# Performance work log

Measured on AMD Instinct MI355X. Metric: run time of the kernel, lower is better.

## Reference

```python
import jax, jax.numpy as jnp
import numpy as np

N_NODES = 200000
N_EDGES = 3200000
N_GRAPHS = 4096
IN_CH = 78
H1, H2, OUT_DIM = 64, 128, 128


def setup_inputs() -> dict:
    key = jax.random.key(0)
    ks = jax.random.split(key, 10)
    x = jax.random.normal(ks[0], (N_NODES, IN_CH), dtype=jnp.float32)
    edge_index = jax.random.randint(ks[1], (2, N_EDGES), 0, N_NODES, dtype=jnp.int64)
    batch = jnp.sort(jax.random.randint(ks[2], (N_NODES,), 0, N_GRAPHS, dtype=jnp.int64))
    # GCNConv weights (PyG: lin has no bias by default; conv bias added after aggregation)
    def glorot(k, fan_in, fan_out):
        lim = jnp.sqrt(6.0 / (fan_in + fan_out)).astype(jnp.float32)
        return jax.random.uniform(k, (fan_in, fan_out), jnp.float32, -lim, lim)
    W1 = glorot(ks[3], IN_CH, H1)
    b1 = jnp.zeros((H1,), jnp.float32)
    W2 = glorot(ks[4], H1, H2)
    b2 = jnp.zeros((H2,), jnp.float32)
    fc_w = glorot(ks[5], H2, OUT_DIM)
    fc_b = jnp.zeros((OUT_DIM,), jnp.float32)
    return {"x": x, "edge_index": edge_index, "batch": batch,
            "W1": W1, "b1": b1, "W2": W2, "b2": b2, "fc_w": fc_w, "fc_b": fc_b}


def _gcn_forward(x, edge_index, batch, W1, b1, W2, b2, fc_w, fc_b):
    N = x.shape[0]
    # GCNConv default: add self loops, symmetric deg^-1/2 normalization
    self_loops = jnp.arange(N, dtype=edge_index.dtype)
    src = jnp.concatenate([edge_index[0], self_loops])  # [E+N]
    dst = jnp.concatenate([edge_index[1], self_loops])  # [E+N]
    deg = jax.ops.segment_sum(jnp.ones_like(dst, dtype=jnp.float32), dst,
                              num_segments=N)  # in-degree incl self loop
    dinv = jnp.where(deg > 0, jax.lax.rsqrt(jnp.maximum(deg, 1.0)), 0.0)
    norm = dinv[src] * dinv[dst]  # [E+N]

    def gcn_layer(h, W, b):
        hw = h @ W                              # transform first (small dims)
        msg = hw[src] * norm[:, None]           # gather + scale  [E+N, F]
        agg = jax.ops.segment_sum(msg, dst, num_segments=N)  # scatter-add
        return agg + b

    h = jax.nn.relu(gcn_layer(x, W1, b1))
    h = jax.nn.relu(gcn_layer(h, W2, b2))
    # global_mean_pool over per-graph segments
    counts = jax.ops.segment_sum(jnp.ones((N,), jnp.float32), batch,
                                 num_segments=N_GRAPHS)
    pooled = jax.ops.segment_sum(h, batch, num_segments=N_GRAPHS)
    pooled = pooled / jnp.maximum(counts, 1.0)[:, None]  # [G, H2]
    return pooled @ fc_w + fc_b                           # [G, OUT_DIM]


def reference(x, edge_index, batch, W1, b1, W2, b2, fc_w, fc_b):
    return _gcn_forward(x, edge_index, batch, W1, b1, W2, b2, fc_w, fc_b)
```

## Files before the change

kernel.cpp:

```cpp
#include <hip/hip_runtime.h>
#include <hip/hip_bf16.h>

#define NN 200000
#define NE 3200000
#define NG 4096
#define INC 78
#define C1 64
#define C2 128
#define ODIM 128
#define KP1 96

#define BSZ 256
#define NBKT 782
#define NBLK 196
#define EPB 16327
#define SCN (NBKT*NBLK)

using bf16 = __hip_bfloat16;
typedef __attribute__((ext_vector_type(8))) short bf16x8;
typedef __attribute__((ext_vector_type(4))) float f32x4;

static inline size_t alignup(size_t x) { return (x + 255) & ~size_t(255); }

__device__ __forceinline__ float bflo(unsigned u) { return __uint_as_float(u << 16); }
__device__ __forceinline__ float bfhi(unsigned u) { return __uint_as_float(u & 0xffff0000u); }
__device__ __forceinline__ unsigned short f2bf(float f) {
    __hip_bfloat16 h = __float2bfloat16(f);
    return *reinterpret_cast<unsigned short*>(&h);
}

__global__ void hist1_kernel(const int* __restrict__ dst, int* __restrict__ histM) {
    __shared__ int lh[NBKT];
    for (int j = threadIdx.x; j < NBKT; j += 256) lh[j] = 0;
    __syncthreads();
    int e0 = blockIdx.x * EPB;
    int e1 = e0 + EPB; if (e1 > NE) e1 = NE;
    for (int e = e0 + threadIdx.x; e < e1; e += 256)
        atomicAdd(&lh[((unsigned)dst[e]) >> 8], 1);
    __syncthreads();
    for (int j = threadIdx.x; j < NBKT; j += 256)
        histM[j * NBLK + blockIdx.x] = lh[j];
}

__global__ void scan1_kernel(int* __restrict__ data, int* __restrict__ bsum, int n) {
    __shared__ int tmp[256];
    int tid = threadIdx.x, gid = blockIdx.x * 256 + tid;
    int v = (gid < n) ? data[gid] : 0;
    tmp[tid] = v;
    __syncthreads();
    for (int off = 1; off < 256; off <<= 1) {
        int t = (tid >= off) ? tmp[tid - off] : 0;
        __syncthreads();
        tmp[tid] += t;
        __syncthreads();
    }
    if (gid < n) data[gid] = tmp[tid] - v;
    if (tid == 255) bsum[blockIdx.x] = tmp[255];
}

__global__ void scan2_kernel(int* __restrict__ bsum, int nb) {
    __shared__ int tmp[1024];
    int tid = threadIdx.x;
    int v = (tid < nb) ? bsum[tid] : 0;
    tmp[tid] = v;
    __syncthreads();
    for (int off = 1; off < 1024; off <<= 1) {
        int t = (tid >= off) ? tmp[tid - off] : 0;
        __syncthreads();
        tmp[tid] += t;
        __syncthreads();
    }
    if (tid < nb) bsum[tid] = tmp[tid] - v;
}

__global__ void scatter2_kernel(const int* __restrict__ src, const int* __restrict__ dst,
                                const int* __restrict__ histM, const int* __restrict__ bsum,
                                unsigned* __restrict__ ebuf) {
    __shared__ int lc[NBKT];
    for (int j = threadIdx.x; j < NBKT; j += 256) {
        int idx = j * NBLK + blockIdx.x;
        lc[j] = histM[idx] + bsum[idx >> 8];
    }
    __syncthreads();
    int e0 = blockIdx.x * EPB;
    int e1 = e0 + EPB; if (e1 > NE) e1 = NE;
    for (int e = e0 + threadIdx.x; e < e1; e += 256) {
        int d = dst[e];
        int s = src[e];
        int pos = atomicAdd(&lc[((unsigned)d) >> 8], 1);
        ebuf[pos] = ((unsigned)s << 8) | (unsigned)(d & 255);
    }
}

__global__ __launch_bounds__(256) void degcsr_kernel(
    const unsigned* __restrict__ ebuf, const int* __restrict__ histM,
    const int* __restrict__ bsum, int* __restrict__ rs, float* __restrict__ dinv,
    unsigned* __restrict__ csr) {
    __shared__ int cnt[BSZ];
    __shared__ int pfx[BSZ];
    int b = blockIdx.x;
    int i0 = b * NBLK;
    int s0 = histM[i0] + bsum[i0 >> 8];
    int s1 = NE;
    if (b + 1 < NBKT) {
        int i1 = (b + 1) * NBLK;
        s1 = histM[i1] + bsum[i1 >> 8];
    }
    cnt[threadIdx.x] = 0;
    __syncthreads();
    for (int i = s0 + threadIdx.x; i < s1; i += 256)
        atomicAdd(&cnt[ebuf[i] & 255], 1);
    __syncthreads();
    int v = cnt[threadIdx.x];
    pfx[threadIdx.x] = v;
    __syncthreads();
    for (int off = 1; off < 256; off <<= 1) {
        int t = (threadIdx.x >= off) ? pfx[threadIdx.x - off] : 0;
        __syncthreads();
        pfx[threadIdx.x] += t;
        __syncthreads();
    }
    int myrs = s0 + pfx[threadIdx.x] - v;
    int node = b * BSZ + threadIdx.x;
    if (node < NN) {
        rs[node] = myrs;
        dinv[node] = rsqrtf((float)v + 1.0f);
    }
    if (node == NN) rs[NN] = NE;
    __syncthreads();
    cnt[threadIdx.x] = 0;
    pfx[threadIdx.x] = myrs;
    __syncthreads();
    for (int i = s0 + threadIdx.x; i < s1; i += 256) {
        unsigned rec = ebuf[i];
        int nl = rec & 255;
        int pos = atomicAdd(&cnt[nl], 1);
        csr[pfx[nl] + pos] = rec >> 8;
    }
}

__global__ void convw2_kernel(const float* __restrict__ W1, const float* __restrict__ W2,
                              unsigned short* __restrict__ Wt1, unsigned short* __restrict__ Wt2) {
    int idx = blockIdx.x * 256 + threadIdx.x;
    if (idx < C1 * KP1) {
        int c = idx / KP1, k = idx % KP1;
        Wt1[idx] = f2bf((k < INC) ? W1[k * C1 + c] : 0.f);
    } else {
        int j = idx - C1 * KP1;
        if (j < C2 * C1) {
            int c = j / C1, k = j % C1;
            Wt2[j] = f2bf(W2[k * C2 + c]);
        }
    }
}

__global__ __launch_bounds__(256) void gemm1_mfma(const float* __restrict__ x,
                                                  const unsigned short* __restrict__ Wt1,
                                                  const float* __restrict__ dinv,
                                                  unsigned short* __restrict__ hw1s) {
    int wave = threadIdx.x >> 6, lane = threadIdx.x & 63;
    int r = lane & 15, kg = lane >> 4;
    int row0 = blockIdx.x * 64 + wave * 16;
    const float* arow = x + (size_t)(row0 + r) * INC;
    bf16x8 a[3];
    #pragma unroll
    for (int t = 0; t < 3; ++t) {
        union { bf16x8 v; unsigned short u[8]; } tmp;
        #pragma unroll
        for (int j = 0; j < 8; ++j) {
            int k = t * 32 + kg * 8 + j;
            tmp.u[j] = (k < INC) ? f2bf(arow[k]) : (unsigned short)0;
        }
        a[t] = tmp.v;
    }
    float dsc[4];
    #pragma unroll
    for (int i = 0; i < 4; ++i) dsc[i] = dinv[row0 + kg * 4 + i];
    #pragma unroll
    for (int nt = 0; nt < 4; ++nt) {
        const unsigned short* wrow = Wt1 + (size_t)(nt * 16 + r) * KP1 + kg * 8;
        bf16x8 b0 = *(const bf16x8*)(wrow);
        bf16x8 b1 = *(const bf16x8*)(wrow + 32);
        bf16x8 b2 = *(const bf16x8*)(wrow + 64);
        f32x4 acc = {0.f, 0.f, 0.f, 0.f};
        acc = __builtin_amdgcn_mfma_f32_16x16x32_bf16(a[0], b0, acc, 0, 0, 0);
        acc = __builtin_amdgcn_mfma_f32_16x16x32_bf16(a[1], b1, acc, 0, 0, 0);
        acc = __builtin_amdgcn_mfma_f32_16x16x32_bf16(a[2], b2, acc, 0, 0, 0);
        unsigned short* cb = hw1s + (size_t)(row0 + kg * 4) * C1 + nt * 16 + r;
        #pragma unroll
        for (int i = 0; i < 4; ++i) cb[(size_t)i * C1] = f2bf(acc[i] * dsc[i]);
    }
}

template <int EP>
__global__ __launch_bounds__(256) void agg_csr_kernel(
    const unsigned* __restrict__ csr, const int* __restrict__ rs,
    const float* __restrict__ dinv, const unsigned short* __restrict__ vin,
    const float* __restrict__ bias, unsigned short* __restrict__ vout) {
    int node = blockIdx.x * 32 + (threadIdx.x >> 3);
    int l = threadIdx.x & 7;
    int c0 = l * 8;
    int start = rs[node], len = rs[node + 1] - start;
    float a0 = 0.f, a1 = 0.f, a2 = 0.f, a3 = 0.f;
    float a4 = 0.f, a5 = 0.f, a6 = 0.f, a7 = 0.f;
    int e = 0;
    for (; e + 2 <= len; e += 2) {
        unsigned sA = csr[start + e], sB = csr[start + e + 1];
        uint4 ra = *(const uint4*)(vin + (size_t)sA * 64 + c0);
        uint4 rb = *(const uint4*)(vin + (size_t)sB * 64 + c0);
        a0 += bflo(ra.x) + bflo(rb.x);
        a1 += bfhi(ra.x) + bfhi(rb.x);
        a2 += bflo(ra.y) + bflo(rb.y);
        a3 += bfhi(ra.y) + bfhi(rb.y);
        a4 += bflo(ra.z) + bflo(rb.z);
        a5 += bfhi(ra.z) + bfhi(rb.z);
        a6 += bflo(ra.w) + bflo(rb.w);
        a7 += bfhi(ra.w) + bfhi(rb.w);
    }
    if (e < len) {
        unsigned sA = csr[start + e];
        uint4 ra = *(const uint4*)(vin + (size_t)sA * 64 + c0);
        a0 += bflo(ra.x); a1 += bfhi(ra.x);
        a2 += bflo(ra.y); a3 += bfhi(ra.y);
        a4 += bflo(ra.z); a5 += bfhi(ra.z);
        a6 += bflo(ra.w); a7 += bfhi(ra.w);
    }
    uint4 sv = *(const uint4*)(vin + (size_t)node * 64 + c0);
    a0 += bflo(sv.x); a1 += bfhi(sv.x);
    a2 += bflo(sv.y); a3 += bfhi(sv.y);
    a4 += bflo(sv.z); a5 += bfhi(sv.z);
    a6 += bflo(sv.w); a7 += bfhi(sv.w);
    float d = dinv[node];
    a0 *= d; a1 *= d; a2 *= d; a3 *= d; a4 *= d; a5 *= d; a6 *= d; a7 *= d;
    if (EP == 1) {
        a0 = fmaxf(a0 + bias[c0 + 0], 0.f) * d;
        a1 = fmaxf(a1 + bias[c0 + 1], 0.f) * d;
        a2 = fmaxf(a2 + bias[c0 + 2], 0.f) * d;
        a3 = fmaxf(a3 + bias[c0 + 3], 0.f) * d;
        a4 = fmaxf(a4 + bias[c0 + 4], 0.f) * d;
        a5 = fmaxf(a5 + bias[c0 + 5], 0.f) * d;
        a6 = fmaxf(a6 + bias[c0 + 6], 0.f) * d;
        a7 = fmaxf(a7 + bias[c0 + 7], 0.f) * d;
    }
    uint4 o;
    o.x = (unsigned)f2bf(a0) | ((unsigned)f2bf(a1) << 16);
    o.y = (unsigned)f2bf(a2) | ((unsigned)f2bf(a3) << 16);
    o.z = (unsigned)f2bf(a4) | ((unsigned)f2bf(a5) << 16);
    o.w = (unsigned)f2bf(a6) | ((unsigned)f2bf(a7) << 16);
    *(uint4*)(vout + (size_t)node * 64 + c0) = o;
}

__global__ __launch_bounds__(256) void gemm2_mfma(const unsigned short* __restrict__ aggH,
                                                  const unsigned short* __restrict__ Wt2,
                                                  const float* __restrict__ b2,
                                                  unsigned short* __restrict__ h2) {
    int wave = threadIdx.x >> 6, lane = threadIdx.x & 63;
    int r = lane & 15, kg = lane >> 4;
    int row0 = blockIdx.x * 64 + wave * 16;
    const unsigned short* arow = aggH + (size_t)(row0 + r) * 64 + kg * 8;
    bf16x8 a0 = *(const bf16x8*)(arow);
    bf16x8 a1 = *(const bf16x8*)(arow + 32);
    #pragma unroll
    for (int nt = 0; nt < 8; ++nt) {
        const unsigned short* wrow = Wt2 + (size_t)(nt * 16 + r) * C1 + kg * 8;
        bf16x8 b0 = *(const bf16x8*)(wrow);
        bf16x8 b1 = *(const bf16x8*)(wrow + 32);
        f32x4 acc = {0.f, 0.f, 0.f, 0.f};
        acc = __builtin_amdgcn_mfma_f32_16x16x32_bf16(a0, b0, acc, 0, 0, 0);
        acc = __builtin_amdgcn_mfma_f32_16x16x32_bf16(a1, b1, acc, 0, 0, 0);
        int col = nt * 16 + r;
        float bb = b2[col];
        unsigned short* cb = h2 + (size_t)(row0 + kg * 4) * C2 + col;
        #pragma unroll
        for (int i = 0; i < 4; ++i) cb[(size_t)i * C2] = f2bf(fmaxf(acc[i] + bb, 0.f));
    }
}

__device__ __forceinline__ int lbound(const int* __restrict__ a, int n, int key) {
    int lo = 0, hi = n;
    while (lo < hi) {
        int mid = (lo + hi) >> 1;
        if (a[mid] < key) lo = mid + 1; else hi = mid;
    }
    return lo;
}

__global__ __launch_bounds__(256) void pool_fc_kernel(const unsigned short* __restrict__ h2,
                                                      const int* __restrict__ batch,
                                                      const float* __restrict__ fcw,
                                                      const float* __restrict__ fcb,
                                                      float* __restrict__ out) {
    __shared__ float ps[512];
    __shared__ float pr[128];
    int g = blockIdx.x;
    int lo = lbound(batch, NN, g);
    int hi = lbound(batch, NN, g + 1);
    int cnt = hi - lo;
    int rg = threadIdx.x >> 6;
    int p = threadIdx.x & 63;
    float s0 = 0.f, s1 = 0.f;
    for (int r = lo + rg; r < hi; r += 4) {
        unsigned v = *(const unsigned*)(h2 + (size_t)r * C2 + p * 2);
        s0 += bflo(v);
        s1 += bfhi(v);
    }
    ps[threadIdx.x * 2 + 0] = s0;
    ps[threadIdx.x * 2 + 1] = s1;
    __syncthreads();
    if (threadIdx.x < 64) {
        float inv = 1.0f / (float)((cnt > 0) ? cnt : 1);
        int t = threadIdx.x;
        float r0 = 0.f, r1 = 0.f;
        #pragma unroll
        for (int k = 0; k < 4; ++k) {
            r0 += ps[(k * 64 + t) * 2 + 0];
            r1 += ps[(k * 64 + t) * 2 + 1];
        }
        pr[2 * t + 0] = r0 * inv;
        pr[2 * t + 1] = r1 * inv;
    }
    __syncthreads();
    if (threadIdx.x < 128) {
        int o = threadIdx.x;
        float acc = fcb[o];
        #pragma unroll 8
        for (int k = 0; k < C2; ++k) acc += pr[k] * fcw[k * ODIM + o];
        out[(size_t)g * ODIM + o] = acc;
    }
}

extern "C" void kernel_launch(void* const* d_in, const int* in_sizes, int n_in,
                              void* d_out, int out_size, void* d_ws, size_t ws_size,
                              hipStream_t stream) {
    const float* x   = (const float*)d_in[0];
    const int*   ei  = (const int*)d_in[1];
    const int*   bat = (const int*)d_in[2];
    const float* W1  = (const float*)d_in[3];
    const float* b1  = (const float*)d_in[4];
    const float* W2  = (const float*)d_in[5];
    const float* b2  = (const float*)d_in[6];
    const float* fcw = (const float*)d_in[7];
    const float* fcb = (const float*)d_in[8];
    float* out = (float*)d_out;

    const int* src = ei;
    const int* dst = ei + NE;

    char* ws = (char*)d_ws;
    int* histM   = (int*)ws;            ws += alignup((size_t)SCN * 4);
    int* bsum    = (int*)ws;            ws += alignup(1024 * 4);
    int* rs      = (int*)ws;            ws += alignup((size_t)(NN + 1) * 4);
    float* dinv  = (float*)ws;          ws += alignup((size_t)NN * 4);
    unsigned short* Wt1 = (unsigned short*)ws;  ws += alignup((size_t)C1 * KP1 * 2);
    unsigned short* Wt2 = (unsigned short*)ws;  ws += alignup((size_t)C2 * C1 * 2);
    unsigned short* hw1s = (unsigned short*)ws; ws += alignup((size_t)NN * C1 * 2);
    unsigned short* aggH = hw1s;
    unsigned* ebuf = (unsigned*)ws;     ws += alignup((size_t)NE * 4);
    unsigned* csr  = (unsigned*)ws;     ws += alignup((size_t)NE * 4);
    unsigned short* h1s = (unsigned short*)ws;  ws += alignup((size_t)NN * C1 * 2);
    unsigned short* h2 = (unsigned short*)ebuf;

    hist1_kernel<<<NBLK, 256, 0, stream>>>(dst, histM);
    const int SCB = (SCN + 255) / 256;
    scan1_kernel<<<SCB, 256, 0, stream>>>(histM, bsum, SCN);
    scan2_kernel<<<1, 1024, 0, stream>>>(bsum, SCB);
    scatter2_kernel<<<NBLK, 256, 0, stream>>>(src, dst, histM, bsum, ebuf);

    degcsr_kernel<<<NBKT, 256, 0, stream>>>(ebuf, histM, bsum, rs, dinv, csr);

    convw2_kernel<<<(C1 * KP1 + C2 * C1 + 255) / 256, 256, 0, stream>>>(W1, W2, Wt1, Wt2);

    gemm1_mfma<<<NN / 64, 256, 0, stream>>>(x, Wt1, dinv, hw1s);
    agg_csr_kernel<1><<<NN / 32, 256, 0, stream>>>(csr, rs, dinv, hw1s, b1, h1s);

    agg_csr_kernel<2><<<NN / 32, 256, 0, stream>>>(csr, rs, dinv, h1s, b1, aggH);
    gemm2_mfma<<<NN / 64, 256, 0, stream>>>(aggH, Wt2, b2, h2);

    pool_fc_kernel<<<NG, 256, 0, stream>>>(h2, bat, fcw, fcb, out);
}
```

Before: 304.4 us.

## Fuse layer-2 aggregation into GEMM, build CSR in place, stage x via LDS

```diff
diff --git a/kernel.cpp b/kernel.cpp
--- a/kernel.cpp
+++ b/kernel.cpp
@@ -15,6 +15,7 @@
 #define NBLK 196
 #define EPB 16327
 #define SCN (NBKT*NBLK)
+#define MAXREC 12288
 
 using bf16 = __hip_bfloat16;
 typedef __attribute__((ext_vector_type(8))) short bf16x8;
@@ -75,7 +76,7 @@
 
 __global__ void scatter2_kernel(const int* __restrict__ src, const int* __restrict__ dst,
                                 const int* __restrict__ histM, const int* __restrict__ bsum,
-                                unsigned* __restrict__ ebuf) {
+                                unsigned* __restrict__ ecsr) {
     __shared__ int lc[NBKT];
     for (int j = threadIdx.x; j < NBKT; j += 256) {
         int idx = j * NBLK + blockIdx.x;
@@ -88,16 +89,16 @@
         int d = dst[e];
         int s = src[e];
         int pos = atomicAdd(&lc[((unsigned)d) >> 8], 1);
-        ebuf[pos] = ((unsigned)s << 8) | (unsigned)(d & 255);
+        ecsr[pos] = ((unsigned)s << 8) | (unsigned)(d & 255);
     }
 }
 
 __global__ __launch_bounds__(256) void degcsr_kernel(
-    const unsigned* __restrict__ ebuf, const int* __restrict__ histM,
-    const int* __restrict__ bsum, int* __restrict__ rs, float* __restrict__ dinv,
-    unsigned* __restrict__ csr) {
+    const int* __restrict__ histM, const int* __restrict__ bsum,
+    int* __restrict__ rs, float* __restrict__ dinv, unsigned* __restrict__ ecsr) {
     __shared__ int cnt[BSZ];
     __shared__ int pfx[BSZ];
+    __shared__ unsigned recs[MAXREC];
     int b = blockIdx.x;
     int i0 = b * NBLK;
     int s0 = histM[i0] + bsum[i0 >> 8];
@@ -106,10 +107,13 @@
         int i1 = (b + 1) * NBLK;
         s1 = histM[i1] + bsum[i1 >> 8];
     }
+    int nrec = s1 - s0;
+    if (nrec > MAXREC) nrec = MAXREC;
     cnt[threadIdx.x] = 0;
-    __syncthreads();
-    for (int i = s0 + threadIdx.x; i < s1; i += 256)
-        atomicAdd(&cnt[ebuf[i] & 255], 1);
+    for (int i = threadIdx.x; i < nrec; i += 256) recs[i] = ecsr[s0 + i];
+    __syncthreads();
+    for (int i = threadIdx.x; i < nrec; i += 256)
+        atomicAdd(&cnt[recs[i] & 255], 1);
     __syncthreads();
     int v = cnt[threadIdx.x];
     pfx[threadIdx.x] = v;
@@ -131,11 +135,11 @@
     cnt[threadIdx.x] = 0;
     pfx[threadIdx.x] = myrs;
     __syncthreads();
-    for (int i = s0 + threadIdx.x; i < s1; i += 256) {
-        unsigned rec = ebuf[i];
+    for (int i = threadIdx.x; i < nrec; i += 256) {
+        unsigned rec = recs[i];
         int nl = rec & 255;
         int pos = atomicAdd(&cnt[nl], 1);
-        csr[pfx[nl] + pos] = rec >> 8;
+        ecsr[pfx[nl] + pos] = rec >> 8;
     }
 }
 
@@ -158,10 +162,20 @@
                                                   const unsigned short* __restrict__ Wt1,
                                                   const float* __restrict__ dinv,
                                                   unsigned short* __restrict__ hw1s) {
+    __shared__ float xs[64 * INC];
+    const float4* gsrc = (const float4*)(x + (size_t)blockIdx.x * 64 * INC);
+    float4* ldst = (float4*)xs;
+    #pragma unroll
+    for (int t = 0; t < 5; ++t) {
+        int i = t * 256 + threadIdx.x;
+        if (i < (64 * INC) / 4) ldst[i] = gsrc[i];
+    }
+    __syncthreads();
     int wave = threadIdx.x >> 6, lane = threadIdx.x & 63;
     int r = lane & 15, kg = lane >> 4;
+    int lrow = wave * 16 + r;
     int row0 = blockIdx.x * 64 + wave * 16;
-    const float* arow = x + (size_t)(row0 + r) * INC;
+    const float* arow = xs + lrow * INC;
     bf16x8 a[3];
     #pragma unroll
     for (int t = 0; t < 3; ++t) {
@@ -192,8 +206,41 @@
     }
 }
 
-template <int EP>
-__global__ __launch_bounds__(256) void agg_csr_kernel(
+__device__ __forceinline__ void gather_node(
+    const unsigned* __restrict__ csr, int start, int len,
+    const unsigned short* __restrict__ vin, int c0,
+    float& a0, float& a1, float& a2, float& a3,
+    float& a4, float& a5, float& a6, float& a7) {
+    int e = 0;
+    for (; e + 4 <= len; e += 4) {
+        unsigned s0 = csr[start + e + 0];
+        unsigned s1 = csr[start + e + 1];
+        unsigned s2 = csr[start + e + 2];
+        unsigned s3 = csr[start + e + 3];
+        uint4 r0 = *(const uint4*)(vin + (size_t)s0 * 64 + c0);
+        uint4 r1 = *(const uint4*)(vin + (size_t)s1 * 64 + c0);
+        uint4 r2 = *(const uint4*)(vin + (size_t)s2 * 64 + c0);
+        uint4 r3 = *(const uint4*)(vin + (size_t)s3 * 64 + c0);
+        a0 += (bflo(r0.x) + bflo(r1.x)) + (bflo(r2.x) + bflo(r3.x));
+        a1 += (bfhi(r0.x) + bfhi(r1.x)) + (bfhi(r2.x) + bfhi(r3.x));
+        a2 += (bflo(r0.y) + bflo(r1.y)) + (bflo(r2.y) + bflo(r3.y));
+        a3 += (bfhi(r0.y) + bfhi(r1.y)) + (bfhi(r2.y) + bfhi(r3.y));
+        a4 += (bflo(r0.z) + bflo(r1.z)) + (bflo(r2.z) + bflo(r3.z));
+        a5 += (bfhi(r0.z) + bfhi(r1.z)) + (bfhi(r2.z) + bfhi(r3.z));
+        a6 += (bflo(r0.w) + bflo(r1.w)) + (bflo(r2.w) + bflo(r3.w));
+        a7 += (bfhi(r0.w) + bfhi(r1.w)) + (bfhi(r2.w) + bfhi(r3.w));
+    }
+    for (; e < len; ++e) {
+        unsigned s = csr[start + e];
+        uint4 ra = *(const uint4*)(vin + (size_t)s * 64 + c0);
+        a0 += bflo(ra.x); a1 += bfhi(ra.x);
+        a2 += bflo(ra.y); a3 += bfhi(ra.y);
+        a4 += bflo(ra.z); a5 += bfhi(ra.z);
+        a6 += bflo(ra.w); a7 += bfhi(ra.w);
+    }
+}
+
+__global__ __launch_bounds__(256) void agg1_kernel(
     const unsigned* __restrict__ csr, const int* __restrict__ rs,
     const float* __restrict__ dinv, const unsigned short* __restrict__ vin,
     const float* __restrict__ bias, unsigned short* __restrict__ vout) {
@@ -201,47 +248,22 @@
     int l = threadIdx.x & 7;
     int c0 = l * 8;
     int start = rs[node], len = rs[node + 1] - start;
-    float a0 = 0.f, a1 = 0.f, a2 = 0.f, a3 = 0.f;
-    float a4 = 0.f, a5 = 0.f, a6 = 0.f, a7 = 0.f;
-    int e = 0;
-    for (; e + 2 <= len; e += 2) {
-        unsigned sA = csr[start + e], sB = csr[start + e + 1];
-        uint4 ra = *(const uint4*)(vin + (size_t)sA * 64 + c0);
-        uint4 rb = *(const uint4*)(vin + (size_t)sB * 64 + c0);
-        a0 += bflo(ra.x) + bflo(rb.x);
-        a1 += bfhi(ra.x) + bfhi(rb.x);
-        a2 += bflo(ra.y) + bflo(rb.y);
-        a3 += bfhi(ra.y) + bfhi(rb.y);
-        a4 += bflo(ra.z) + bflo(rb.z);
-        a5 += bfhi(ra.z) + bfhi(rb.z);
-        a6 += bflo(ra.w) + bflo(rb.w);
-        a7 += bfhi(ra.w) + bfhi(rb.w);
-    }
-    if (e < len) {
-        unsigned sA = csr[start + e];
-        uint4 ra = *(const uint4*)(vin + (size_t)sA * 64 + c0);
-        a0 += bflo(ra.x); a1 += bfhi(ra.x);
-        a2 += bflo(ra.y); a3 += bfhi(ra.y);
-        a4 += bflo(ra.z); a5 += bfhi(ra.z);
-        a6 += bflo(ra.w); a7 += bfhi(ra.w);
-    }
+    float a0 = 0.f, a1 = 0.f, a2 = 0.f, a3 = 0.f, a4 = 0.f, a5 = 0.f, a6 = 0.f, a7 = 0.f;
+    gather_node(csr, start, len, vin, c0, a0, a1, a2, a3, a4, a5, a6, a7);
     uint4 sv = *(const uint4*)(vin + (size_t)node * 64 + c0);
     a0 += bflo(sv.x); a1 += bfhi(sv.x);
     a2 += bflo(sv.y); a3 += bfhi(sv.y);
     a4 += bflo(sv.z); a5 += bfhi(sv.z);
     a6 += bflo(sv.w); a7 += bfhi(sv.w);
     float d = dinv[node];
-    a0 *= d; a1 *= d; a2 *= d; a3 *= d; a4 *= d; a5 *= d; a6 *= d; a7 *= d;
-    if (EP == 1) {
-        a0 = fmaxf(a0 + bias[c0 + 0], 0.f) * d;
-        a1 = fmaxf(a1 + bias[c0 + 1], 0.f) * d;
-        a2 = fmaxf(a2 + bias[c0 + 2], 0.f) * d;
-        a3 = fmaxf(a3 + bias[c0 + 3], 0.f) * d;
-        a4 = fmaxf(a4 + bias[c0 + 4], 0.f) * d;
-        a5 = fmaxf(a5 + bias[c0 + 5], 0.f) * d;
-        a6 = fmaxf(a6 + bias[c0 + 6], 0.f) * d;
-        a7 = fmaxf(a7 + bias[c0 + 7], 0.f) * d;
-    }
+    a0 = fmaxf(a0 * d + bias[c0 + 0], 0.f) * d;
+    a1 = fmaxf(a1 * d + bias[c0 + 1], 0.f) * d;
+    a2 = fmaxf(a2 * d + bias[c0 + 2], 0.f) * d;
+    a3 = fmaxf(a3 * d + bias[c0 + 3], 0.f) * d;
+    a4 = fmaxf(a4 * d + bias[c0 + 4], 0.f) * d;
+    a5 = fmaxf(a5 * d + bias[c0 + 5], 0.f) * d;
+    a6 = fmaxf(a6 * d + bias[c0 + 6], 0.f) * d;
+    a7 = fmaxf(a7 * d + bias[c0 + 7], 0.f) * d;
     uint4 o;
     o.x = (unsigned)f2bf(a0) | ((unsigned)f2bf(a1) << 16);
     o.y = (unsigned)f2bf(a2) | ((unsigned)f2bf(a3) << 16);
@@ -250,16 +272,42 @@
     *(uint4*)(vout + (size_t)node * 64 + c0) = o;
 }
 
-__global__ __launch_bounds__(256) void gemm2_mfma(const unsigned short* __restrict__ aggH,
-                                                  const unsigned short* __restrict__ Wt2,
-                                                  const float* __restrict__ b2,
-                                                  unsigned short* __restrict__ h2) {
+__global__ __launch_bounds__(256) void agg2g_mfma(
+    const unsigned* __restrict__ csr, const int* __restrict__ rs,
+    const float* __restrict__ dinv, const unsigned short* __restrict__ h1s,
+    const unsigned short* __restrict__ Wt2, const float* __restrict__ b2,
+    unsigned short* __restrict__ h2) {
+    __shared__ unsigned short A[64 * 72];
+    int grp = threadIdx.x >> 3;
+    int l = threadIdx.x & 7;
+    int c0 = l * 8;
+    #pragma unroll
+    for (int half = 0; half < 2; ++half) {
+        int nl = grp + half * 32;
+        int node = blockIdx.x * 64 + nl;
+        int start = rs[node], len = rs[node + 1] - start;
+        float a0 = 0.f, a1 = 0.f, a2 = 0.f, a3 = 0.f, a4 = 0.f, a5 = 0.f, a6 = 0.f, a7 = 0.f;
+        gather_node(csr, start, len, h1s, c0, a0, a1, a2, a3, a4, a5, a6, a7);
+        uint4 sv = *(const uint4*)(h1s + (size_t)node * 64 + c0);
+        a0 += bflo(sv.x); a1 += bfhi(sv.x);
+        a2 += bflo(sv.y); a3 += bfhi(sv.y);
+        a4 += bflo(sv.z); a5 += bfhi(sv.z);
+        a6 += bflo(sv.w); a7 += bfhi(sv.w);
+        float d = dinv[node];
+        uint4 o;
+        o.x = (unsigned)f2bf(a0 * d) | ((unsigned)f2bf(a1 * d) << 16);
+        o.y = (unsigned)f2bf(a2 * d) | ((unsigned)f2bf(a3 * d) << 16);
+        o.z = (unsigned)f2bf(a4 * d) | ((unsigned)f2bf(a5 * d) << 16);
+        o.w = (unsigned)f2bf(a6 * d) | ((unsigned)f2bf(a7 * d) << 16);
+        *(uint4*)(A + nl * 72 + c0) = o;
+    }
+    __syncthreads();
     int wave = threadIdx.x >> 6, lane = threadIdx.x & 63;
     int r = lane & 15, kg = lane >> 4;
+    int lrow = wave * 16 + r;
     int row0 = blockIdx.x * 64 + wave * 16;
-    const unsigned short* arow = aggH + (size_t)(row0 + r) * 64 + kg * 8;
-    bf16x8 a0 = *(const bf16x8*)(arow);
-    bf16x8 a1 = *(const bf16x8*)(arow + 32);
+    bf16x8 a0 = *(const bf16x8*)(A + lrow * 72 + kg * 8);
+    bf16x8 a1 = *(const bf16x8*)(A + lrow * 72 + 32 + kg * 8);
     #pragma unroll
     for (int nt = 0; nt < 8; ++nt) {
         const unsigned short* wrow = Wt2 + (size_t)(nt * 16 + r) * C1 + kg * 8;
@@ -354,27 +402,24 @@
     unsigned short* Wt1 = (unsigned short*)ws;  ws += alignup((size_t)C1 * KP1 * 2);
     unsigned short* Wt2 = (unsigned short*)ws;  ws += alignup((size_t)C2 * C1 * 2);
     unsigned short* hw1s = (unsigned short*)ws; ws += alignup((size_t)NN * C1 * 2);
-    unsigned short* aggH = hw1s;
-    unsigned* ebuf = (unsigned*)ws;     ws += alignup((size_t)NE * 4);
-    unsigned* csr  = (unsigned*)ws;     ws += alignup((size_t)NE * 4);
+    unsigned* ecsr = (unsigned*)ws;     ws += alignup((size_t)NE * 4);
     unsigned short* h1s = (unsigned short*)ws;  ws += alignup((size_t)NN * C1 * 2);
-    unsigned short* h2 = (unsigned short*)ebuf;
+    unsigned short* h2 = (unsigned short*)ws;   ws += alignup((size_t)NN * C2 * 2);
 
     hist1_kernel<<<NBLK, 256, 0, stream>>>(dst, histM);
     const int SCB = (SCN + 255) / 256;
     scan1_kernel<<<SCB, 256, 0, stream>>>(histM, bsum, SCN);
     scan2_kernel<<<1, 1024, 0, stream>>>(bsum, SCB);
-    scatter2_kernel<<<NBLK, 256, 0, stream>>>(src, dst, histM, bsum, ebuf);
-
-    degcsr_kernel<<<NBKT, 256, 0, stream>>>(ebuf, histM, bsum, rs, dinv, csr);
+    scatter2_kernel<<<NBLK, 256, 0, stream>>>(src, dst, histM, bsum, ecsr);
+
+    degcsr_kernel<<<NBKT, 256, 0, stream>>>(histM, bsum, rs, dinv, ecsr);
 
     convw2_kernel<<<(C1 * KP1 + C2 * C1 + 255) / 256, 256, 0, stream>>>(W1, W2, Wt1, Wt2);
 
     gemm1_mfma<<<NN / 64, 256, 0, stream>>>(x, Wt1, dinv, hw1s);
-    agg_csr_kernel<1><<<NN / 32, 256, 0, stream>>>(csr, rs, dinv, hw1s, b1, h1s);
-
-    agg_csr_kernel<2><<<NN / 32, 256, 0, stream>>>(csr, rs, dinv, h1s, b1, aggH);
-    gemm2_mfma<<<NN / 64, 256, 0, stream>>>(aggH, Wt2, b2, h2);
+    agg1_kernel<<<NN / 32, 256, 0, stream>>>(ecsr, rs, dinv, hw1s, b1, h1s);
+
+    agg2g_mfma<<<NN / 64, 256, 0, stream>>>(ecsr, rs, dinv, h1s, Wt2, b2, h2);
 
     pool_fc_kernel<<<NG, 256, 0, stream>>>(h2, bat, fcw, fcb, out);
 }
```

After: 299.7 us. No clear change (-1.6%).
